# Performance work log

Hardware: AMD Instinct MI355X
Metric: run time of the kernel (lower is better)

Reference implementation:

```python
import jax, jax.numpy as jnp
import numpy as np


def _linear_sum_assignment(cost):
    """Jonker-Volgenant shortest-augmenting-path LSAP (matches scipy.optimize.linear_sum_assignment).
    cost: [n, m] float array (rectangular ok). Returns (row_ind, col_ind) with len = min(n, m)."""
    cost = np.asarray(cost, dtype=np.float64)
    transposed = cost.shape[0] > cost.shape[1]
    if transposed:
        cost = cost.T
    n, m = cost.shape
    u = np.zeros(n)
    v = np.zeros(m)
    path = np.full(m, -1, dtype=np.int64)
    col4row = np.full(n, -1, dtype=np.int64)
    row4col = np.full(m, -1, dtype=np.int64)
    for cur_row in range(n):
        shortest = np.full(m, np.inf)
        SR = np.zeros(n, dtype=bool)
        SC = np.zeros(m, dtype=bool)
        i = cur_row
        min_val = 0.0
        sink = -1
        while sink == -1:
            SR[i] = True
            idx = np.where(~SC)[0]  # unscanned columns
            r = min_val + cost[i, idx] - u[i] - v[idx]
            better = r < shortest[idx]
            bidx = idx[better]
            path[bidx] = i
            shortest[bidx] = r[better]
            j = idx[np.argmin(shortest[idx])]
            min_val = shortest[j]
            SC[j] = True
            if row4col[j] == -1:
                sink = j
            else:
                i = row4col[j]
        # dual variable updates
        u[cur_row] += min_val
        others = SR.copy()
        others[cur_row] = False
        oi = np.where(others)[0]
        u[oi] += min_val - shortest[col4row[oi]]
        ci = np.where(SC)[0]
        v[ci] -= min_val - shortest[ci]
        # augment along the alternating path
        j = sink
        while True:
            i = path[j]
            row4col[j] = i
            col4row[i], j = j, col4row[i]
            if i == cur_row:
                break
    if transposed:
        rows = col4row
        cols = np.arange(n, dtype=np.int64)
        order = np.argsort(rows)
        return rows[order], cols[order]
    return np.arange(n, dtype=np.int64), col4row


def setup_inputs() -> dict:
    key = jax.random.key(0)
    k1, k2 = jax.random.split(key)
    N, NUM_CLASSES, T = 8192, 32000, 128
    outputs = jax.random.normal(k1, (N, NUM_CLASSES), dtype=jnp.float32)
    targets = jax.random.randint(k2, (T,), 0, NUM_CLASSES, dtype=jnp.int64)
    return {"outputs": outputs, "targets": targets}


def reference(outputs, targets):
    # C[i, t] = 1 - softmax(outputs)[i, targets[t]]  -> [num_queries, num_targets]
    probs = jax.nn.softmax(outputs, axis=-1)
    C = 1.0 - probs[:, targets]
    row_ind, col_ind = _linear_sum_assignment(np.asarray(jax.device_get(C)))
    return jnp.asarray(row_ind), jnp.asarray(col_ind)
```

## Files before the change

kernel.cpp:

```cpp
#include <hip/hip_runtime.h>
#include <hip/hip_bf16.h>
#include <math.h>

#define NQ 8192
#define NC 32000
#define NT 128
#define SROW 256
#define SLOTC 128

typedef float v4f __attribute__((ext_vector_type(4)));

__global__ __launch_bounds__(256) void build_cost(
    const float* __restrict__ outp, const int* __restrict__ tgt,
    float* __restrict__ C, float* __restrict__ Ccol)
{
  const int row = blockIdx.x;
  const int tid = threadIdx.x;
  const float* x = outp + (size_t)row * NC;

  float m = -INFINITY;
  double s = 0.0;
  const v4f* x4 = (const v4f*)x;
  for (int k = tid; k < NC / 4; k += 256) {
    v4f v = __builtin_nontemporal_load(x4 + k);
    float mv = fmaxf(fmaxf(v.x, v.y), fmaxf(v.z, v.w));
    if (mv > m) { s *= exp((double)(m - mv)); m = mv; }
    s += (double)__expf(v.x - m) + (double)__expf(v.y - m)
       + (double)__expf(v.z - m) + (double)__expf(v.w - m);
  }

  __shared__ float  lsm[4];
  __shared__ double lss[4];
  __shared__ float  bM;
  __shared__ double bS;

  float wm = m;
  #pragma unroll
  for (int off = 32; off; off >>= 1) wm = fmaxf(wm, __shfl_xor(wm, off));
  const int wid = tid >> 6;
  if ((tid & 63) == 0) lsm[wid] = wm;
  __syncthreads();
  if (tid == 0) bM = fmaxf(fmaxf(lsm[0], lsm[1]), fmaxf(lsm[2], lsm[3]));
  __syncthreads();
  const float M = bM;

  double s2 = s * exp((double)m - (double)M);
  #pragma unroll
  for (int off = 32; off; off >>= 1) s2 += __shfl_xor(s2, off);
  if ((tid & 63) == 0) lss[wid] = s2;
  __syncthreads();
  if (tid == 0) bS = lss[0] + lss[1] + lss[2] + lss[3];
  __syncthreads();
  const double S = bS;

  if (tid < NT) {
    const int c = tgt[tid];
    const double p = exp((double)x[c] - (double)M) / S;
    const float cv = 1.0f - (float)p;
    C[(size_t)tid * NQ + row]    = cv;
    Ccol[(size_t)row * NT + tid] = cv;
  }
}

__global__ __launch_bounds__(256) void select_part(
    const float* __restrict__ C, unsigned long long* __restrict__ S1)
{
  __shared__ unsigned long long key[1024];
  const int part = blockIdx.x, t = blockIdx.y, tid = threadIdx.x;
  const float* crow = C + (size_t)t * NQ + part * 1024;
  for (int i = tid; i < 1024; i += 256)
    key[i] = ((unsigned long long)__float_as_uint(crow[i]) << 32)
           | (unsigned)(part * 1024 + i);

  for (int k = 2; k <= 256; k <<= 1)
    for (int jj = k >> 1; jj > 0; jj >>= 1) {
      __syncthreads();
      for (int w = tid; w < 512; w += 256) {
        const int i1 = ((w & ~(jj - 1)) << 1) | (w & (jj - 1));
        const int i2 = i1 | jj;
        const bool up = (((i1 & 255) & k) == 0);
        const unsigned long long a = key[i1], b = key[i2];
        if ((a > b) == up) { key[i1] = b; key[i2] = a; }
      }
    }

  for (int step = 1; step < 4; step <<= 1) {
    const int npairs = 2 / step;
    __syncthreads();
    for (int w = tid; w < npairs * 256; w += 256) {
      const int p = w >> 8, i = w & 255;
      const int a = ((p * 2 * step) << 8) + i;
      const int b = ((p * 2 * step + step) << 8) + 255 - i;
      const unsigned long long ka = key[a], kb = key[b];
      if (ka > kb) key[a] = kb;
    }
    for (int jj = 128; jj > 0; jj >>= 1) {
      __syncthreads();
      for (int w = tid; w < npairs * 128; w += 256) {
        const int p = w >> 7, q = w & 127;
        const int base = (p * 2 * step) << 8;
        const int i1 = base + (((q & ~(jj - 1)) << 1) | (q & (jj - 1)));
        const int i2 = i1 | jj;
        const unsigned long long a = key[i1], b = key[i2];
        if (a > b) { key[i1] = b; key[i2] = a; }
      }
    }
  }
  __syncthreads();
  S1[((size_t)t * 8 + part) * 256 + tid] = key[tid];
}

__global__ __launch_bounds__(256) void select_merge(
    const unsigned long long* __restrict__ S1, unsigned long long* __restrict__ S)
{
  __shared__ unsigned long long key[2048];
  const int t = blockIdx.x, tid = threadIdx.x;
  for (int i = tid; i < 2048; i += 256) key[i] = S1[(size_t)t * 2048 + i];

  for (int step = 1; step < 8; step <<= 1) {
    const int npairs = 4 / step;
    __syncthreads();
    for (int w = tid; w < npairs * 256; w += 256) {
      const int p = w >> 8, i = w & 255;
      const int a = ((p * 2 * step) << 8) + i;
      const int b = ((p * 2 * step + step) << 8) + 255 - i;
      const unsigned long long ka = key[a], kb = key[b];
      if (ka > kb) key[a] = kb;
    }
    for (int jj = 128; jj > 0; jj >>= 1) {
      __syncthreads();
      for (int w = tid; w < npairs * 128; w += 256) {
        const int p = w >> 7, q = w & 127;
        const int base = (p * 2 * step) << 8;
        const int i1 = base + (((q & ~(jj - 1)) << 1) | (q & (jj - 1)));
        const int i2 = i1 | jj;
        const unsigned long long a = key[i1], b = key[i2];
        if (a > b) { key[i1] = b; key[i2] = a; }
      }
    }
  }
  __syncthreads();
  S[(size_t)t * SROW + tid] = key[tid];
}

__device__ __forceinline__ int rl_i32(int v, int l) {
  return __builtin_amdgcn_readlane(v, l);
}
__device__ __forceinline__ double rl_f64(double v, int l) {
  union { double d; int i[2]; } a; a.d = v;
  union { int i[2]; double d; } r;
  r.i[0] = __builtin_amdgcn_readlane(a.i[0], l);
  r.i[1] = __builtin_amdgcn_readlane(a.i[1], l);
  return r.d;
}
__device__ __forceinline__ unsigned long long rl_u64(unsigned long long v, int l) {
  union { unsigned long long q; int i[2]; } a; a.q = v;
  union { int i[2]; unsigned long long q; } r;
  r.i[0] = __builtin_amdgcn_readlane(a.i[0], l);
  r.i[1] = __builtin_amdgcn_readlane(a.i[1], l);
  return r.q;
}

template <int CTRL>
__device__ __forceinline__ void dpp_lexmin(double& cr, int& cj) {
  union { double d; int i[2]; } a, r;
  a.d = cr;
  r.i[0] = __builtin_amdgcn_update_dpp(0, a.i[0], CTRL, 0xF, 0xF, true);
  r.i[1] = __builtin_amdgcn_update_dpp(0, a.i[1], CTRL, 0xF, 0xF, true);
  const int oj = __builtin_amdgcn_update_dpp(0, cj, CTRL, 0xF, 0xF, true);
  const double ov = r.d;
  if (ov < cr || (ov == cr && oj < cj)) { cr = ov; cj = oj; }
}

__global__ __launch_bounds__(64) void lsap_solve(
    const float* __restrict__ Ccol, const unsigned long long* __restrict__ S,
    int* __restrict__ outi)
{
  const int lane = threadIdx.x;

  __shared__ float  Clds[NT][SLOTC];
  __shared__ double u[NT];
  __shared__ unsigned long long abm[NQ / 64];
  __shared__ short col4row[NT];

  int    acolA = -1, acolB = -1;
  int    arowA = -1, arowB = -1;
  int    apathA = -1, apathB = -1;
  double avA = 0.0, avB = 0.0;
  double ashA = 0.0, ashB = 0.0;
  double afzA = 0.0, afzB = 0.0;
  bool   ascA = false, ascB = false;
  int    nA = 0;

  unsigned long long candA = 0ull, candB = 0ull;
  int curA = 0, curB = 0;

  u[lane] = 0.0;        u[64 + lane] = 0.0;
  col4row[lane] = -1;   col4row[64 + lane] = -1;
  abm[lane] = 0ull;     abm[64 + lane] = 0ull;

  for (int cur = 0; cur < NT; ++cur) {
    ashA = INFINITY; ashB = INFINITY; ascA = false; ascB = false;
    double ub_r = INFINITY; int ub_j = 0x7fffffff, ub_i = -1;
    int icur = cur; double minval = 0.0;
    int sink = -1, sinkpath = -1;

    while (sink < 0) {
      const double u_i = u[icur];
      const bool actA = (lane < nA) && !ascA;
      const bool actB = (64 + lane < nA) && !ascB;
      float cA = 0.f, cB = 0.f;
      if (actA) cA = Clds[icur][(lane + icur) & 127];
      if (actB) cB = Clds[icur][(64 + lane + icur) & 127];

      unsigned long long kk = (icur < 64) ? rl_u64(candA, icur)
                                          : rl_u64(candB, icur - 64);
      if (kk == 0ull) {
        int pos = (icur < 64) ? rl_i32(curA, icur) : rl_i32(curB, icur - 64);
        for (;;) {
          const unsigned long long k = S[(size_t)icur * SROW + pos + lane];
          const int j = (int)(k & 0xffffffffu);
          const bool asg = (abm[j >> 6] >> (j & 63)) & 1ull;
          const unsigned long long bal = __ballot(!asg);
          if (bal) {
            const int f = __builtin_ctzll(bal);
            kk = rl_u64(k, f);
            pos += f;
            break;
          }
          pos += 64;
        }
        if (lane == (icur & 63)) {
          if (icur < 64) { candA = kk; curA = pos; }
          else           { candB = kk; curB = pos; }
        }
      }
      {
        const int    jU = (int)(kk & 0xffffffffu);
        const double cU = (double)__uint_as_float((unsigned)(kk >> 32));
        const double rU = ((minval + cU) - u_i) - 0.0;
        if (rU < ub_r || (rU == ub_r && jU < ub_j)) { ub_r = rU; ub_j = jU; ub_i = icur; }
      }

      double cr = INFINITY; int cj = 0x7fffffff;
      if (actA) {
        const double r = ((minval + (double)cA) - u_i) - avA;
        if (r < ashA) { ashA = r; apathA = icur; }
        cr = ashA; cj = acolA;
      }
      if (actB) {
        const double r = ((minval + (double)cB) - u_i) - avB;
        if (r < ashB) { ashB = r; apathB = icur; }
        if (ashB < cr || (ashB == cr && acolB < cj)) { cr = ashB; cj = acolB; }
      }
      dpp_lexmin<0xB1>(cr, cj);
      dpp_lexmin<0x4E>(cr, cj);
      dpp_lexmin<0x141>(cr, cj);
      dpp_lexmin<0x140>(cr, cj);
      {
        double bv = rl_f64(cr, 0);  int bj = rl_i32(cj, 0);
        const double g1 = rl_f64(cr, 16); const int j1 = rl_i32(cj, 16);
        if (g1 < bv || (g1 == bv && j1 < bj)) { bv = g1; bj = j1; }
        const double g2 = rl_f64(cr, 32); const int j2 = rl_i32(cj, 32);
        if (g2 < bv || (g2 == bv && j2 < bj)) { bv = g2; bj = j2; }
        const double g3 = rl_f64(cr, 48); const int j3 = rl_i32(cj, 48);
        if (g3 < bv || (g3 == bv && j3 < bj)) { bv = g3; bj = j3; }
        cr = bv; cj = bj;
      }

      if (cr < ub_r || (cr == ub_r && cj < ub_j)) {
        minval = cr;
        const bool mineA = actA && (ashA == cr) && (acolA == cj);
        const bool mineB = actB && (ashB == cr) && (acolB == cj);
        const unsigned long long bal = __ballot(mineA || mineB);
        const int ln  = (int)__builtin_ctzll(bal);
        const int isB = rl_i32(mineB ? 1 : 0, ln);
        if (lane == ln) {
          if (isB) { ascB = true; afzB = cr; }
          else     { ascA = true; afzA = cr; }
        }
        icur = isB ? rl_i32(arowB, ln) : rl_i32(arowA, ln);
      } else {
        minval = ub_r;
        sink = ub_j; sinkpath = ub_i;
      }
    }

    const int nAold = nA;
    const float fc0 = Ccol[(size_t)sink * NT + lane];
    const float fc1 = Ccol[(size_t)sink * NT + 64 + lane];

    if (lane == 0) u[cur] += minval;
    if (ascA) { u[arowA] += minval - afzA; avA -= (minval - afzA); }
    if (ascB) { u[arowB] += minval - afzB; avB -= (minval - afzB); }

    {
      int j = sink, i = sinkpath;
      if (lane == (nAold & 63)) {
        if (nAold < 64) { acolA = sink; avA = 0.0; arowA = i; }
        else            { acolB = sink; avB = 0.0; arowB = i; }
      }
      if (lane == 0) abm[sink >> 6] |= 1ull << (sink & 63);
      nA = nAold + 1;
      for (;;) {
        const int jn = col4row[i];
        if (lane == 0) col4row[i] = (short)j;
        if (i == cur) break;
        j = jn;
        const bool hA = (acolA == j);
        const bool hB = (acolB == j);
        const unsigned long long bal = __ballot(hA || hB);
        const int ln = (int)__builtin_ctzll(bal);
        const int isB = rl_i32(hB ? 1 : 0, ln);
        const int ni = isB ? rl_i32(apathB, ln) : rl_i32(apathA, ln);
        if (lane == ln) { if (isB) arowB = ni; else arowA = ni; }
        i = ni;
      }
    }

    if ((int)(candA & 0xffffffffu) == sink) candA = 0ull;
    if ((int)(candB & 0xffffffffu) == sink) candB = 0ull;

    Clds[lane][(nAold + lane) & 127]           = fc0;
    Clds[64 + lane][(nAold + 64 + lane) & 127] = fc1;
  }

  for (int t = lane; t < NT; t += 64) {
    const int q = col4row[t];
    int rank = 0;
    for (int k = 0; k < NT; ++k) rank += (col4row[k] < q);
    outi[rank]      = q;
    outi[NT + rank] = t;
  }
}

extern "C" void kernel_launch(void* const* d_in, const int* in_sizes, int n_in,
                              void* d_out, int out_size, void* d_ws, size_t ws_size,
                              hipStream_t stream) {
  (void)in_sizes; (void)n_in; (void)out_size; (void)ws_size;
  const float* outputs = (const float*)d_in[0];
  const int*   targets = (const int*)d_in[1];
  char* ws = (char*)d_ws;
  float* C    = (float*)ws;
  float* Ccol = (float*)(ws + (size_t)NT * NQ * 4);
  unsigned long long* S1 =
      (unsigned long long*)(ws + (size_t)NT * NQ * 8);
  unsigned long long* S =
      (unsigned long long*)(ws + (size_t)NT * NQ * 8 + (size_t)NT * 8 * 256 * 8);
  int* out = (int*)d_out;

  build_cost<<<NQ, 256, 0, stream>>>(outputs, targets, C, Ccol);
  select_part<<<dim3(8, NT), 256, 0, stream>>>(C, S1);
  select_merge<<<NT, 256, 0, stream>>>(S1, S);
  lsap_solve<<<1, 64, 0, stream>>>(Ccol, S, out);
}
```

Measured before the change: 406.4 us.

## Keep LSAP duals and col4row in registers, simplify argmin reduction

```diff
diff --git a/kernel.cpp b/kernel.cpp
--- a/kernel.cpp
+++ b/kernel.cpp
@@ -162,14 +162,12 @@
 }
 
 template <int CTRL>
-__device__ __forceinline__ void dpp_lexmin(double& cr, int& cj) {
+__device__ __forceinline__ double dpp_min_f64(double cr) {
   union { double d; int i[2]; } a, r;
   a.d = cr;
   r.i[0] = __builtin_amdgcn_update_dpp(0, a.i[0], CTRL, 0xF, 0xF, true);
   r.i[1] = __builtin_amdgcn_update_dpp(0, a.i[1], CTRL, 0xF, 0xF, true);
-  const int oj = __builtin_amdgcn_update_dpp(0, cj, CTRL, 0xF, 0xF, true);
-  const double ov = r.d;
-  if (ov < cr || (ov == cr && oj < cj)) { cr = ov; cj = oj; }
+  return fmin(cr, r.d);
 }
 
 __global__ __launch_bounds__(64) void lsap_solve(
@@ -179,9 +177,9 @@
   const int lane = threadIdx.x;
 
   __shared__ float  Clds[NT][SLOTC];
-  __shared__ double u[NT];
+  __shared__ double du[NT];
   __shared__ unsigned long long abm[NQ / 64];
-  __shared__ short col4row[NT];
+  __shared__ short col4row_s[NT];
 
   int    acolA = -1, acolB = -1;
   int    arowA = -1, arowB = -1;
@@ -192,12 +190,14 @@
   bool   ascA = false, ascB = false;
   int    nA = 0;
 
-  unsigned long long candA = 0ull, candB = 0ull;
-  int curA = 0, curB = 0;
-
-  u[lane] = 0.0;        u[64 + lane] = 0.0;
-  col4row[lane] = -1;   col4row[64 + lane] = -1;
-  abm[lane] = 0ull;     abm[64 + lane] = 0ull;
+  double uA = 0.0, uB = 0.0;
+  int    c4rA = -1, c4rB = -1;
+  unsigned long long candA, candB;
+  int    curA = 0, curB = 0;
+
+  abm[lane] = 0ull;  abm[64 + lane] = 0ull;
+  candA = S[(size_t)lane * SROW];
+  candB = S[(size_t)(64 + lane) * SROW];
 
   for (int cur = 0; cur < NT; ++cur) {
     ashA = INFINITY; ashB = INFINITY; ascA = false; ascB = false;
@@ -206,7 +206,7 @@
     int sink = -1, sinkpath = -1;
 
     while (sink < 0) {
-      const double u_i = u[icur];
+      const double u_i = (icur < 64) ? rl_f64(uA, icur) : rl_f64(uB, icur - 64);
       const bool actA = (lane < nA) && !ascA;
       const bool actB = (64 + lane < nA) && !ascB;
       float cA = 0.f, cB = 0.f;
@@ -242,39 +242,49 @@
         if (rU < ub_r || (rU == ub_r && jU < ub_j)) { ub_r = rU; ub_j = jU; ub_i = icur; }
       }
 
-      double cr = INFINITY; int cj = 0x7fffffff;
       if (actA) {
         const double r = ((minval + (double)cA) - u_i) - avA;
         if (r < ashA) { ashA = r; apathA = icur; }
-        cr = ashA; cj = acolA;
       }
       if (actB) {
         const double r = ((minval + (double)cB) - u_i) - avB;
         if (r < ashB) { ashB = r; apathB = icur; }
-        if (ashB < cr || (ashB == cr && acolB < cj)) { cr = ashB; cj = acolB; }
-      }
-      dpp_lexmin<0xB1>(cr, cj);
-      dpp_lexmin<0x4E>(cr, cj);
-      dpp_lexmin<0x141>(cr, cj);
-      dpp_lexmin<0x140>(cr, cj);
-      {
-        double bv = rl_f64(cr, 0);  int bj = rl_i32(cj, 0);
-        const double g1 = rl_f64(cr, 16); const int j1 = rl_i32(cj, 16);
-        if (g1 < bv || (g1 == bv && j1 < bj)) { bv = g1; bj = j1; }
-        const double g2 = rl_f64(cr, 32); const int j2 = rl_i32(cj, 32);
-        if (g2 < bv || (g2 == bv && j2 < bj)) { bv = g2; bj = j2; }
-        const double g3 = rl_f64(cr, 48); const int j3 = rl_i32(cj, 48);
-        if (g3 < bv || (g3 == bv && j3 < bj)) { bv = g3; bj = j3; }
-        cr = bv; cj = bj;
+      }
+      double cr = actA ? ashA : INFINITY;
+      if (actB) cr = fmin(cr, ashB);
+      cr = dpp_min_f64<0xB1>(cr);
+      cr = dpp_min_f64<0x4E>(cr);
+      cr = dpp_min_f64<0x141>(cr);
+      cr = dpp_min_f64<0x140>(cr);
+      cr = fmin(fmin(rl_f64(cr, 0), rl_f64(cr, 16)),
+                fmin(rl_f64(cr, 32), rl_f64(cr, 48)));
+
+      const bool mA = actA && (ashA == cr);
+      const bool mB = actB && (ashB == cr);
+      const unsigned long long balA = __ballot(mA);
+      const unsigned long long balB = __ballot(mB);
+      int ln = -1, isB = 0, cj = 0x7fffffff;
+      if (__popcll(balA) + __popcll(balB) == 1) {
+        isB = (balA == 0ull);
+        ln  = (int)__builtin_ctzll(balA | balB);
+        cj  = isB ? rl_i32(acolB, ln) : rl_i32(acolA, ln);
+      } else if ((balA | balB) != 0ull) {
+        unsigned long long ba = balA;
+        while (ba) {
+          const int l = (int)__builtin_ctzll(ba); ba &= ba - 1;
+          const int c = rl_i32(acolA, l);
+          if (c < cj) { cj = c; ln = l; isB = 0; }
+        }
+        unsigned long long bb = balB;
+        while (bb) {
+          const int l = (int)__builtin_ctzll(bb); bb &= bb - 1;
+          const int c = rl_i32(acolB, l);
+          if (c < cj) { cj = c; ln = l; isB = 1; }
+        }
       }
 
       if (cr < ub_r || (cr == ub_r && cj < ub_j)) {
         minval = cr;
-        const bool mineA = actA && (ashA == cr) && (acolA == cj);
-        const bool mineB = actB && (ashB == cr) && (acolB == cj);
-        const unsigned long long bal = __ballot(mineA || mineB);
-        const int ln  = (int)__builtin_ctzll(bal);
-        const int isB = rl_i32(mineB ? 1 : 0, ln);
         if (lane == ln) {
           if (isB) { ascB = true; afzB = cr; }
           else     { ascA = true; afzA = cr; }
@@ -290,9 +300,12 @@
     const float fc0 = Ccol[(size_t)sink * NT + lane];
     const float fc1 = Ccol[(size_t)sink * NT + 64 + lane];
 
-    if (lane == 0) u[cur] += minval;
-    if (ascA) { u[arowA] += minval - afzA; avA -= (minval - afzA); }
-    if (ascB) { u[arowB] += minval - afzB; avB -= (minval - afzB); }
+    du[lane] = 0.0; du[64 + lane] = 0.0;
+    if (ascA) { du[arowA] = minval - afzA; avA -= (minval - afzA); }
+    if (ascB) { du[arowB] = minval - afzB; avB -= (minval - afzB); }
+    uA += du[lane];
+    uB += du[64 + lane];
+    if (lane == (cur & 63)) { if (cur < 64) uA += minval; else uB += minval; }
 
     {
       int j = sink, i = sinkpath;
@@ -303,17 +316,17 @@
       if (lane == 0) abm[sink >> 6] |= 1ull << (sink & 63);
       nA = nAold + 1;
       for (;;) {
-        const int jn = col4row[i];
-        if (lane == 0) col4row[i] = (short)j;
+        const int jn = (i < 64) ? rl_i32(c4rA, i) : rl_i32(c4rB, i - 64);
+        if (lane == (i & 63)) { if (i < 64) c4rA = j; else c4rB = j; }
         if (i == cur) break;
         j = jn;
         const bool hA = (acolA == j);
         const bool hB = (acolB == j);
         const unsigned long long bal = __ballot(hA || hB);
-        const int ln = (int)__builtin_ctzll(bal);
-        const int isB = rl_i32(hB ? 1 : 0, ln);
-        const int ni = isB ? rl_i32(apathB, ln) : rl_i32(apathA, ln);
-        if (lane == ln) { if (isB) arowB = ni; else arowA = ni; }
+        const int ln2 = (int)__builtin_ctzll(bal);
+        const int isB2 = rl_i32(hB ? 1 : 0, ln2);
+        const int ni = isB2 ? rl_i32(apathB, ln2) : rl_i32(apathA, ln2);
+        if (lane == ln2) { if (isB2) arowB = ni; else arowA = ni; }
         i = ni;
       }
     }
@@ -325,10 +338,12 @@
     Clds[64 + lane][(nAold + 64 + lane) & 127] = fc1;
   }
 
+  col4row_s[lane]      = (short)c4rA;
+  col4row_s[64 + lane] = (short)c4rB;
   for (int t = lane; t < NT; t += 64) {
-    const int q = col4row[t];
+    const int q = col4row_s[t];
     int rank = 0;
-    for (int k = 0; k < NT; ++k) rank += (col4row[k] < q);
+    for (int k = 0; k < NT; ++k) rank += (col4row_s[k] < q);
     outi[rank]      = q;
     outi[NT + rank] = t;
   }
```

After: 337.9 us. 1.2x faster.
